# Optimization experiments

Hardware: AMD Instinct MI355X
Metric: run time of the kernel (lower is better)

Reference implementation:

```python
import jax, jax.numpy as jnp
import numpy as np

B, N, C = 8, 2048, 1024
SPARSITY = 0.8
K_KEEP = int(N * SPARSITY)  # 1638
NEG = 1e10


def setup_inputs() -> dict:
    key = jax.random.key(0)
    ks = jax.random.split(key, 7)
    s = 1.0 / np.sqrt(C)
    return {
        "x": jax.random.normal(ks[0], (B, N, C), dtype=jnp.float32),
        "Wq": jax.random.uniform(ks[1], (C, C), dtype=jnp.float32, minval=-s, maxval=s),
        "bq": jax.random.uniform(ks[2], (C,), dtype=jnp.float32, minval=-s, maxval=s),
        "Wk": jax.random.uniform(ks[3], (C, C), dtype=jnp.float32, minval=-s, maxval=s),
        "bk": jax.random.uniform(ks[4], (C,), dtype=jnp.float32, minval=-s, maxval=s),
        "Wv": jax.random.uniform(ks[5], (C, C), dtype=jnp.float32, minval=-s, maxval=s),
        "bv": jax.random.uniform(ks[6], (C,), dtype=jnp.float32, minval=-s, maxval=s),
    }


def reference(x, Wq, bq, Wk, bk, Wv, bv):
    # Linear projections (torch Linear: y = x @ W.T + b)
    Q = jnp.einsum("bnc,dc->bnd", x, Wq) + bq
    Kt = jnp.einsum("bnc,dc->bnd", x, Wk) + bk
    V = jnp.einsum("bnc,dc->bnd", x, Wv) + bv
    attn = jnp.einsum("bnd,bmd->bnm", Q, Kt) / jnp.sqrt(jnp.float32(C))  # [B,N,N]
    _, idx = jax.lax.top_k(attn, K_KEEP)  # idx: [B,N,K_KEEP]
    bI = jnp.arange(B)[:, None, None]
    nI = jnp.arange(N)[None, :, None]
    mask = jnp.zeros_like(attn).at[bI, nI, idx].set(1.0)
    attn = attn * mask - NEG * (1.0 - mask)
    attn = jax.nn.softmax(attn, axis=-1)
    return jnp.einsum("bnm,bmd->bnd", attn, V)
```

## Files before the change

kernel.cpp:

```cpp
#include <hip/hip_runtime.h>

typedef _Float16 f16;
typedef __attribute__((ext_vector_type(8))) _Float16 f16x8;
typedef __attribute__((ext_vector_type(4))) _Float16 f16x4;
typedef __attribute__((ext_vector_type(4))) float f32x4;

constexpr int BB = 8;
constexpr int NN = 2048;
constexpr int CC = 1024;
constexpr int MTOT = BB * NN;
constexpr int KKEEP = 1638;

__device__ __forceinline__ void gl_lds16(const void* g, void* l) {
  __builtin_amdgcn_global_load_lds((__attribute__((address_space(1))) void*)g,
                                   (__attribute__((address_space(3))) void*)l,
                                   16, 0, 0);
}

constexpr int X4 = MTOT * CC / 4;
constexpr int W4 = CC * CC / 4;
__global__ __launch_bounds__(256) void cvt_all(
    const float* __restrict__ x, const float* __restrict__ Wq,
    const float* __restrict__ Wk, const float* __restrict__ Wv,
    f16* __restrict__ xb, f16* __restrict__ wqkv) {
  int i = blockIdx.x * 256 + threadIdx.x;
  const float* s;
  f16* d;
  if (i < X4) { s = x; d = xb; }
  else if (i < X4 + W4) { i -= X4; s = Wq; d = wqkv; }
  else if (i < X4 + 2 * W4) { i -= X4 + W4; s = Wk; d = wqkv + CC * CC; }
  else { i -= X4 + 2 * W4; s = Wv; d = wqkv + 2 * CC * CC; }
  float4 f = ((const float4*)s)[i];
  f16x4 o = {(f16)f.x, (f16)f.y, (f16)f.z, (f16)f.w};
  ((f16x4*)d)[i] = o;
}

#define STAGE_A(buf, h, tt)                                              \
  {                                                                      \
    gl_lds16(gA + (size_t)((h) * 128) * lda + (tt) * 64,                 \
             lA + (buf) * 16384 + (h) * 8192);                           \
    gl_lds16(gA + (size_t)((h) * 128 + 8) * lda + (tt) * 64,             \
             lA + (buf) * 16384 + (h) * 8192 + 512);                     \
  }
#define STAGE_B(buf, h, tt)                                              \
  {                                                                      \
    gl_lds16(gB + (size_t)((h) * 128) * ldb + (tt) * 64,                 \
             lB + (buf) * 16384 + (h) * 8192);                           \
    gl_lds16(gB + (size_t)((h) * 128 + 8) * ldb + (tt) * 64,             \
             lB + (buf) * 16384 + (h) * 8192 + 512);                     \
  }

#define MFMA_Q(qm, qn)                                                   \
  {                                                                      \
    __builtin_amdgcn_s_setprio(1);                                       \
    _Pragma("unroll") for (int kk = 0; kk < 2; kk++)                     \
    _Pragma("unroll") for (int ii = 0; ii < 4; ii++)                     \
    _Pragma("unroll") for (int jj = 0; jj < 2; jj++)                     \
        acc[(qm) * 4 + ii][(qn) * 2 + jj] =                              \
            __builtin_amdgcn_mfma_f32_16x16x32_f16(                      \
                av[kk][ii], bv[kk][(qn) * 2 + jj],                       \
                acc[(qm) * 4 + ii][(qn) * 2 + jj], 0, 0, 0);             \
    __builtin_amdgcn_s_setprio(0);                                       \
  }

template <int MODE>
__global__ __launch_bounds__(512, 2) void gemm_bt(
    const f16* __restrict__ A, const f16* __restrict__ B,
    const float* __restrict__ b0, const float* __restrict__ b1,
    const float* __restrict__ b2, void* __restrict__ Cout,
    void* __restrict__ Cout2, int K, int lda, int ldb, int ldc, float scale,
    long strideA, long strideB, long strideC) {
  const f16* Ab = A + (size_t)blockIdx.z * strideA;
  const f16* Bbp = B + (size_t)blockIdx.z * strideB;

  const int bm = blockIdx.x * 256;
  const int bn = blockIdx.y * 256;
  const int tid = threadIdx.x;
  const int wave = tid >> 6;
  const int lane = tid & 63;
  const int wy = wave >> 2;
  const int wx = wave & 3;

  __shared__ __attribute__((aligned(16))) f16 As[2 * 256 * 64];
  __shared__ __attribute__((aligned(16))) f16 Bs[2 * 256 * 64];

  f32x4 acc[8][4];
#pragma unroll
  for (int i = 0; i < 8; i++)
#pragma unroll
    for (int j = 0; j < 4; j++) acc[i][j] = (f32x4){0.f, 0.f, 0.f, 0.f};

  const int srow = wave * 16 + (lane >> 3);
  const int gsrc = ((lane & 7) ^ ((lane >> 3) & 7)) * 8;
  const f16* gA = Ab + (size_t)(bm + srow) * lda + gsrc;
  const f16* gB = Bbp + (size_t)(bn + srow) * ldb + gsrc;
  f16* lA = As + wave * 1024 + lane * 8;
  f16* lB = Bs + wave * 1024 + lane * 8;

  const int NT = K >> 6;

  STAGE_A(0, 0, 0);
  STAGE_B(0, 0, 0);
  STAGE_A(0, 1, 0);
  STAGE_B(0, 1, 0);
  if (NT > 1) {
    STAGE_A(1, 0, 1);
    STAGE_B(1, 0, 1);
    asm volatile("s_waitcnt vmcnt(8)" ::: "memory");
  } else {
    asm volatile("s_waitcnt vmcnt(4)" ::: "memory");
  }
  __builtin_amdgcn_s_barrier();

  const int id = lane & 15;
  const int q = lane >> 4;
  const int g0 = (q ^ (lane & 7)) * 8;
  const int g1 = ((q + 4) ^ (lane & 7)) * 8;
  const int aoff = (wy * 64 + id) * 64;
  const int boff = (wx * 32 + id) * 64;

#pragma unroll 2
  for (int t = 0; t < NT; ++t) {
    const int cur = t & 1;
    const f16* Ac = As + cur * 16384;
    const f16* Bc = Bs + cur * 16384;
    f16x8 av[2][4];
    f16x8 bv[2][4];

#pragma unroll
    for (int ii = 0; ii < 4; ii++) {
      av[0][ii] = *(const f16x8*)(Ac + ii * 1024 + aoff + g0);
      av[1][ii] = *(const f16x8*)(Ac + ii * 1024 + aoff + g1);
    }
#pragma unroll
    for (int jj = 0; jj < 2; jj++) {
      bv[0][jj] = *(const f16x8*)(Bc + jj * 1024 + boff + g0);
      bv[1][jj] = *(const f16x8*)(Bc + jj * 1024 + boff + g1);
    }
    if (t + 1 < NT) STAGE_A(cur ^ 1, 1, t + 1);
    __builtin_amdgcn_s_barrier();
    MFMA_Q(0, 0);
    if (t + 1 < NT) asm volatile("s_waitcnt vmcnt(6)" ::: "memory");
    else            asm volatile("s_waitcnt vmcnt(0)" ::: "memory");
    __builtin_amdgcn_s_barrier();

#pragma unroll
    for (int jj = 0; jj < 2; jj++) {
      bv[0][2 + jj] = *(const f16x8*)(Bc + (128 + jj * 16) * 64 + boff + g0);
      bv[1][2 + jj] = *(const f16x8*)(Bc + (128 + jj * 16) * 64 + boff + g1);
    }
    if (t + 1 < NT) STAGE_B(cur ^ 1, 1, t + 1);
    __builtin_amdgcn_s_barrier();
    MFMA_Q(0, 1);
    __builtin_amdgcn_s_barrier();

#pragma unroll
    for (int ii = 0; ii < 4; ii++) {
      av[0][ii] = *(const f16x8*)(Ac + (128 + ii * 16) * 64 + aoff + g0);
      av[1][ii] = *(const f16x8*)(Ac + (128 + ii * 16) * 64 + aoff + g1);
    }
    if (t + 2 < NT) STAGE_A(cur, 0, t + 2);
    __builtin_amdgcn_s_barrier();
    MFMA_Q(1, 0);
    __builtin_amdgcn_s_barrier();

    if (t + 2 < NT) STAGE_B(cur, 0, t + 2);
    __builtin_amdgcn_s_barrier();
    MFMA_Q(1, 1);
    if (t + 2 < NT)      asm volatile("s_waitcnt vmcnt(8)" ::: "memory");
    else if (t + 1 < NT) asm volatile("s_waitcnt vmcnt(4)" ::: "memory");
    __builtin_amdgcn_s_barrier();
  }

#pragma unroll
  for (int i = 0; i < 8; i++) {
    const int row0 = bm + (i >> 2) * 128 + wy * 64 + (i & 3) * 16 + q * 4;
#pragma unroll
    for (int j = 0; j < 4; j++) {
      const int col = bn + (j >> 1) * 128 + wx * 32 + (j & 1) * 16 + id;
      if (MODE == 0) {
        float* C = (float*)Cout + (size_t)blockIdx.z * strideC;
#pragma unroll
        for (int r = 0; r < 4; r++)
          C[(size_t)(row0 + r) * ldc + col] = acc[i][j][r] * scale;
      } else {
        if (bn < 2048) {
          f16* C = (f16*)Cout;
          const float* bias = (bn < 1024) ? b0 : (b1 - 1024);
          const float bb = bias[col];
#pragma unroll
          for (int r = 0; r < 4; r++)
            C[(size_t)(row0 + r) * 2048 + col] = (f16)(acc[i][j][r] + bb);
        } else {
          f16* C = (f16*)Cout2;
          const float bb = b2[col - 2048];
          f16x4 o;
#pragma unroll
          for (int r = 0; r < 4; r++) o[r] = (f16)(acc[i][j][r] + bb);
          *(f16x4*)(C + (size_t)(col - 2048) * MTOT + row0) = o;
        }
      }
    }
  }
}

__global__ __launch_bounds__(256) void topk_softmax_kernel(
    const float* __restrict__ S, f16* __restrict__ P) {
  const size_t row = blockIdx.x;
  const float* srow = S + row * 2048;
  f16* prow = P + row * 2048;
  const int t = threadIdx.x;
  const int lane = t & 63;
  const int wave = t >> 6;

  float v[8];
  float4 f0 = ((const float4*)srow)[2 * t];
  float4 f1 = ((const float4*)srow)[2 * t + 1];
  v[0] = f0.x; v[1] = f0.y; v[2] = f0.z; v[3] = f0.w;
  v[4] = f1.x; v[5] = f1.y; v[6] = f1.z; v[7] = f1.w;

  __shared__ float wlo[4], whi[4];
  __shared__ float wf[4];
  __shared__ int wagg[4];
  __shared__ int hist[2048];
  __shared__ float cval[128];
  __shared__ int cidx[128];
  __shared__ int cnum;
  __shared__ int sh_thr, sh_want;

  float lo = v[0], hi = v[0];
#pragma unroll
  for (int j = 1; j < 8; j++) { lo = fminf(lo, v[j]); hi = fmaxf(hi, v[j]); }
#pragma unroll
  for (int off = 32; off > 0; off >>= 1) {
    lo = fminf(lo, __shfl_xor(lo, off, 64));
    hi = fmaxf(hi, __shfl_xor(hi, off, 64));
  }
  if (lane == 0) { wlo[wave] = lo; whi[wave] = hi; }
  if (t == 0) cnum = 0;
  ((int4*)hist)[2 * t] = (int4){0, 0, 0, 0};
  ((int4*)hist)[2 * t + 1] = (int4){0, 0, 0, 0};
  __syncthreads();
  lo = fminf(fminf(wlo[0], wlo[1]), fminf(wlo[2], wlo[3]));
  hi = fmaxf(fmaxf(whi[0], whi[1]), fmaxf(whi[2], whi[3]));

  if (hi == lo) {
    const float w = 1.0f / (float)KKEEP;
    f16x8 o;
#pragma unroll
    for (int j = 0; j < 8; j++) o[j] = (f16)((t * 8 + j < KKEEP) ? w : 0.f);
    *(f16x8*)(prow + t * 8) = o;
    return;
  }

  const float qs = 2048.0f / (hi - lo);
  int key[8];
#pragma unroll
  for (int j = 0; j < 8; j++) {
    int k = (int)((v[j] - lo) * qs);
    key[j] = (k > 2047) ? 2047 : k;
  }
#pragma unroll
  for (int j = 0; j < 8; j++) atomicAdd(&hist[key[j]], 1);
  __syncthreads();

  int4 h0 = ((const int4*)hist)[2 * t];
  int4 h1 = ((const int4*)hist)[2 * t + 1];
  int h[8] = {h0.x, h0.y, h0.z, h0.w, h1.x, h1.y, h1.z, h1.w};
  int s[8];
  s[7] = h[7];
#pragma unroll
  for (int j = 6; j >= 0; j--) s[j] = s[j + 1] + h[j];
  const int partial = s[0];
  int sfx = partial;
#pragma unroll
  for (int off = 1; off < 64; off <<= 1) {
    int o = __shfl_down(sfx, off, 64);
    sfx += (lane + off < 64) ? o : 0;
  }
  if (lane == 0) wagg[wave] = sfx;
  __syncthreads();
  int hiw = 0;
#pragma unroll
  for (int w = 0; w < 4; w++) hiw += (w > wave) ? wagg[w] : 0;
  const int base = (sfx - partial) + hiw;
#pragma unroll
  for (int j = 0; j < 8; j++) {
    const int cum = s[j] + base;
    const int above = cum - h[j];
    if (cum >= KKEEP && above < KKEEP) {
      sh_thr = 8 * t + j;
      sh_want = KKEEP - above;
    }
  }
  __syncthreads();
  const int thr = sh_thr;
  const int wantin = sh_want;

#pragma unroll
  for (int j = 0; j < 8; j++) {
    if (key[j] == thr) {
      int slot = atomicAdd(&cnum, 1);
      if (slot < 128) { cval[slot] = v[j]; cidx[slot] = t * 8 + j; }
    }
  }
  __syncthreads();
  const int n = (cnum < 128) ? cnum : 128;

  float e[8];
  float lsum = 0.f;
#pragma unroll
  for (int j = 0; j < 8; j++) {
    bool kept;
    if (key[j] > thr) {
      kept = true;
    } else if (key[j] < thr) {
      kept = false;
    } else {
      const int myidx = t * 8 + j;
      int rank = 0;
      for (int c = 0; c < n; c++) {
        const float cv = cval[c];
        rank += (cv > v[j] || (cv == v[j] && cidx[c] < myidx)) ? 1 : 0;
      }
      kept = rank < wantin;
    }
    e[j] = kept ? __expf(v[j] - hi) : 0.f;
    lsum += e[j];
  }
#pragma unroll
  for (int off = 32; off > 0; off >>= 1) lsum += __shfl_xor(lsum, off, 64);
  if (lane == 0) wf[wave] = lsum;
  __syncthreads();
  const float inv = 1.0f / (wf[0] + wf[1] + wf[2] + wf[3]);

  f16x8 o;
#pragma unroll
  for (int j = 0; j < 8; j++) o[j] = (f16)(e[j] * inv);
  *(f16x8*)(prow + t * 8) = o;
}

extern "C" void kernel_launch(void* const* d_in, const int* in_sizes, int n_in,
                              void* d_out, int out_size, void* d_ws, size_t ws_size,
                              hipStream_t stream) {
  (void)in_sizes; (void)n_in; (void)out_size; (void)ws_size;
  const float* x = (const float*)d_in[0];
  const float* Wq = (const float*)d_in[1];
  const float* bq = (const float*)d_in[2];
  const float* Wk = (const float*)d_in[3];
  const float* bk = (const float*)d_in[4];
  const float* Wv = (const float*)d_in[5];
  const float* bv = (const float*)d_in[6];
  float* out = (float*)d_out;

  char* ws = (char*)d_ws;
  f16* qkb = (f16*)(ws + 0);
  f16* vtb = (f16*)(ws + 67108864);
  float* S = (float*)(ws + 100663296);
  f16* xb = (f16*)(ws + 100663296);
  f16* wqkv = (f16*)(ws + 134217728);
  f16* Pc = (f16*)(ws + 0);

  cvt_all<<<(X4 + 3 * W4 + 255) / 256, 256, 0, stream>>>(x, Wq, Wk, Wv, xb, wqkv);

  gemm_bt<3><<<dim3(MTOT / 256, 3072 / 256, 1), 512, 0, stream>>>(
      xb, wqkv, bq, bk, bv, qkb, vtb, CC, CC, CC, 0, 1.f, 0, 0, 0);

  gemm_bt<0><<<dim3(NN / 256, NN / 256, BB), 512, 0, stream>>>(
      qkb, qkb + 1024, nullptr, nullptr, nullptr, S, nullptr, CC, 2048, 2048, NN,
      1.f / 32.f, (long)NN * 2048, (long)NN * 2048, (long)NN * NN);

  topk_softmax_kernel<<<MTOT, 256, 0, stream>>>(S, Pc);

  gemm_bt<0><<<dim3(NN / 256, CC / 256, BB), 512, 0, stream>>>(
      Pc, vtb, nullptr, nullptr, nullptr, out, nullptr, NN, NN, MTOT, CC, 1.f,
      (long)NN * NN, (long)NN, (long)NN * CC);
}
```

Baseline: 446.1 us.

## Prefetch next tile's LDS fragments into registers across GEMM iterations

```diff
diff --git a/kernel.cpp b/kernel.cpp
--- a/kernel.cpp
+++ b/kernel.cpp
@@ -50,7 +50,28 @@
              lB + (buf) * 16384 + (h) * 8192 + 512);                     \
   }
 
-#define MFMA_Q(qm, qn)                                                   \
+#define RD_A0(dst, buf)                                                  \
+  _Pragma("unroll") for (int ii = 0; ii < 4; ii++) {                     \
+    dst[0][ii] = *(const f16x8*)((buf) + ii * 1024 + aoff + g0);         \
+    dst[1][ii] = *(const f16x8*)((buf) + ii * 1024 + aoff + g1);         \
+  }
+#define RD_A1(dst, buf)                                                  \
+  _Pragma("unroll") for (int ii = 0; ii < 4; ii++) {                     \
+    dst[0][ii] = *(const f16x8*)((buf) + (128 + ii * 16) * 64 + aoff + g0); \
+    dst[1][ii] = *(const f16x8*)((buf) + (128 + ii * 16) * 64 + aoff + g1); \
+  }
+#define RD_B0(dst, buf)                                                  \
+  _Pragma("unroll") for (int jj = 0; jj < 2; jj++) {                     \
+    dst[0][jj] = *(const f16x8*)((buf) + jj * 1024 + boff + g0);         \
+    dst[1][jj] = *(const f16x8*)((buf) + jj * 1024 + boff + g1);         \
+  }
+#define RD_B1(dst, buf)                                                  \
+  _Pragma("unroll") for (int jj = 0; jj < 2; jj++) {                     \
+    dst[0][jj] = *(const f16x8*)((buf) + (128 + jj * 16) * 64 + boff + g0); \
+    dst[1][jj] = *(const f16x8*)((buf) + (128 + jj * 16) * 64 + boff + g1); \
+  }
+
+#define MFMA_Q(qm, qn, A, Bv)                                            \
   {                                                                      \
     __builtin_amdgcn_s_setprio(1);                                       \
     _Pragma("unroll") for (int kk = 0; kk < 2; kk++)                     \
@@ -58,7 +79,7 @@
     _Pragma("unroll") for (int jj = 0; jj < 2; jj++)                     \
         acc[(qm) * 4 + ii][(qn) * 2 + jj] =                              \
             __builtin_amdgcn_mfma_f32_16x16x32_f16(                      \
-                av[kk][ii], bv[kk][(qn) * 2 + jj],                       \
+                A[kk][ii], Bv[kk][jj],                                   \
                 acc[(qm) * 4 + ii][(qn) * 2 + jj], 0, 0, 0);             \
     __builtin_amdgcn_s_setprio(0);                                       \
   }
@@ -97,7 +118,17 @@
   f16* lA = As + wave * 1024 + lane * 8;
   f16* lB = Bs + wave * 1024 + lane * 8;
 
+  const int id = lane & 15;
+  const int q = lane >> 4;
+  const int g0 = (q ^ (lane & 7)) * 8;
+  const int g1 = ((q + 4) ^ (lane & 7)) * 8;
+  const int aoff = (wy * 64 + id) * 64;
+  const int boff = (wx * 32 + id) * 64;
+
   const int NT = K >> 6;
+
+  f16x8 av0[2][4], av1[2][4];
+  f16x8 b0a[2][2], b1a[2][2], b0b[2][2], b1b[2][2];
 
   STAGE_A(0, 0, 0);
   STAGE_B(0, 0, 0);
@@ -106,69 +137,44 @@
   if (NT > 1) {
     STAGE_A(1, 0, 1);
     STAGE_B(1, 0, 1);
-    asm volatile("s_waitcnt vmcnt(8)" ::: "memory");
+    asm volatile("s_waitcnt vmcnt(4)" ::: "memory");
   } else {
-    asm volatile("s_waitcnt vmcnt(4)" ::: "memory");
+    asm volatile("s_waitcnt vmcnt(0)" ::: "memory");
   }
   __builtin_amdgcn_s_barrier();
-
-  const int id = lane & 15;
-  const int q = lane >> 4;
-  const int g0 = (q ^ (lane & 7)) * 8;
-  const int g1 = ((q + 4) ^ (lane & 7)) * 8;
-  const int aoff = (wy * 64 + id) * 64;
-  const int boff = (wx * 32 + id) * 64;
-
-#pragma unroll 2
+  RD_A0(av0, As);
+  RD_B0(b0a, Bs);
+
   for (int t = 0; t < NT; ++t) {
     const int cur = t & 1;
     const f16* Ac = As + cur * 16384;
     const f16* Bc = Bs + cur * 16384;
-    f16x8 av[2][4];
-    f16x8 bv[2][4];
-
-#pragma unroll
-    for (int ii = 0; ii < 4; ii++) {
-      av[0][ii] = *(const f16x8*)(Ac + ii * 1024 + aoff + g0);
-      av[1][ii] = *(const f16x8*)(Ac + ii * 1024 + aoff + g1);
-    }
-#pragma unroll
-    for (int jj = 0; jj < 2; jj++) {
-      bv[0][jj] = *(const f16x8*)(Bc + jj * 1024 + boff + g0);
-      bv[1][jj] = *(const f16x8*)(Bc + jj * 1024 + boff + g1);
-    }
-    if (t + 1 < NT) STAGE_A(cur ^ 1, 1, t + 1);
-    __builtin_amdgcn_s_barrier();
-    MFMA_Q(0, 0);
-    if (t + 1 < NT) asm volatile("s_waitcnt vmcnt(6)" ::: "memory");
-    else            asm volatile("s_waitcnt vmcnt(0)" ::: "memory");
-    __builtin_amdgcn_s_barrier();
-
-#pragma unroll
-    for (int jj = 0; jj < 2; jj++) {
-      bv[0][2 + jj] = *(const f16x8*)(Bc + (128 + jj * 16) * 64 + boff + g0);
-      bv[1][2 + jj] = *(const f16x8*)(Bc + (128 + jj * 16) * 64 + boff + g1);
-    }
-    if (t + 1 < NT) STAGE_B(cur ^ 1, 1, t + 1);
-    __builtin_amdgcn_s_barrier();
-    MFMA_Q(0, 1);
-    __builtin_amdgcn_s_barrier();
-
-#pragma unroll
-    for (int ii = 0; ii < 4; ii++) {
-      av[0][ii] = *(const f16x8*)(Ac + (128 + ii * 16) * 64 + aoff + g0);
-      av[1][ii] = *(const f16x8*)(Ac + (128 + ii * 16) * 64 + aoff + g1);
-    }
-    if (t + 2 < NT) STAGE_A(cur, 0, t + 2);
-    __builtin_amdgcn_s_barrier();
-    MFMA_Q(1, 0);
-    __builtin_amdgcn_s_barrier();
-
-    if (t + 2 < NT) STAGE_B(cur, 0, t + 2);
-    __builtin_amdgcn_s_barrier();
-    MFMA_Q(1, 1);
-    if (t + 2 < NT)      asm volatile("s_waitcnt vmcnt(8)" ::: "memory");
-    else if (t + 1 < NT) asm volatile("s_waitcnt vmcnt(4)" ::: "memory");
+    const f16* An = As + (cur ^ 1) * 16384;
+    const f16* Bn = Bs + (cur ^ 1) * 16384;
+
+    RD_B1(b1a, Bc);
+    RD_B0(b0b, Bc);
+    if (t + 1 < NT) { STAGE_A(cur ^ 1, 1, t + 1); STAGE_B(cur ^ 1, 1, t + 1); }
+    __builtin_amdgcn_s_barrier();
+    MFMA_Q(0, 0, av0, b0a);
+    __builtin_amdgcn_s_barrier();
+
+    RD_A1(av1, Ac);
+    __builtin_amdgcn_s_barrier();
+    MFMA_Q(0, 1, av0, b1a);
+    __builtin_amdgcn_s_barrier();
+
+    RD_B1(b1b, Bc);
+    __builtin_amdgcn_s_barrier();
+    MFMA_Q(1, 0, av1, b0b);
+    asm volatile("s_waitcnt vmcnt(4)" ::: "memory");
+    __builtin_amdgcn_s_barrier();
+
+    if (t + 1 < NT) { RD_A0(av0, An); RD_B0(b0a, Bn); }
+    if (t + 2 < NT) { STAGE_A(cur, 0, t + 2); STAGE_B(cur, 0, t + 2); }
+    __builtin_amdgcn_s_barrier();
+    MFMA_Q(1, 1, av1, b1b);
+    asm volatile("s_waitcnt vmcnt(4)" ::: "memory");
     __builtin_amdgcn_s_barrier();
   }
 
```

Measured after the change: 656.8 us. 47.2% more time.
